# Optimization experiments

Hardware: AMD Instinct MI355X
Metric: run time of the kernel (lower is better)

Reference implementation:

```python
import jax, jax.numpy as jnp
import numpy as np
import math

# Config (matches init_kwargs)
V, D, L, H, KVH, FF = 4054, 1024, 8, 16, 8, 4096
HD = D // H            # 64
NREP = H // KVH        # 2
THETA = 500000.0
EPS = 1e-5
PAD = 4053
B, S = 2, 2048


def setup_inputs() -> dict:
    key = jax.random.key(0)
    ks = jax.random.split(key, 12)
    std = 0.02
    inp = {
        "input_ids": jax.random.randint(ks[0], (B, S), 0, 4050),
        "emb": jax.random.normal(ks[1], (V, D), jnp.float32) * std,
        # Linear weights stored as [in, out] so y = x @ W
        "Wq": jax.random.normal(ks[2], (L, D, H * HD), jnp.float32) * std,
        "Wk": jax.random.normal(ks[3], (L, D, KVH * HD), jnp.float32) * std,
        "Wv": jax.random.normal(ks[4], (L, D, KVH * HD), jnp.float32) * std,
        "Wo": jax.random.normal(ks[5], (L, H * HD, D), jnp.float32) * std,
        "Wg": jax.random.normal(ks[6], (L, D, FF), jnp.float32) * std,
        "Wu": jax.random.normal(ks[7], (L, D, FF), jnp.float32) * std,
        "Wd": jax.random.normal(ks[8], (L, FF, D), jnp.float32) * std,
        "attn_norm_w": jnp.ones((L, D), jnp.float32),
        "ffn_norm_w": jnp.ones((L, D), jnp.float32),
        "final_norm_w": jnp.ones((D,), jnp.float32),
        "lm_head": jax.random.normal(ks[9], (D, V), jnp.float32) * std,
    }
    return inp


def _rms_norm(x, w):
    return x * jax.lax.rsqrt(jnp.mean(x * x, axis=-1, keepdims=True) + EPS) * w


def _rotate_half(x):
    x1, x2 = jnp.split(x, 2, axis=-1)
    return jnp.concatenate([-x2, x1], axis=-1)


def _rope_tables(seq_len):
    inv_freq = 1.0 / (THETA ** (jnp.arange(0, HD, 2, dtype=jnp.float32) / HD))
    t = jnp.arange(seq_len, dtype=jnp.float32)
    freqs = jnp.outer(t, inv_freq)            # [S, HD/2]
    ang = jnp.concatenate([freqs, freqs], -1)  # [S, HD]
    return jnp.cos(ang)[None, None], jnp.sin(ang)[None, None]  # [1,1,S,HD]


def reference(input_ids, emb, Wq, Wk, Wv, Wo, Wg, Wu, Wd,
              attn_norm_w, ffn_norm_w, final_norm_w, lm_head):
    b, s = input_ids.shape
    x = emb[input_ids]                                    # [B,S,D]

    cos, sin = _rope_tables(s)

    # causal mask + pad-key mask (pad tokens cannot be attended to)
    causal = jnp.triu(jnp.full((s, s), -jnp.inf, jnp.float32), k=1)
    pad_bias = jnp.where(input_ids == PAD, -jnp.inf, 0.0)  # [B,S]
    mask = causal[None, None] + pad_bias[:, None, None, :]  # [B,1,S,S]

    scale = 1.0 / math.sqrt(HD)

    def block(h, p):
        wq, wk, wv, wo, wg, wu, wd, anw, fnw = p
        hn = _rms_norm(h, anw)
        q = (hn @ wq).reshape(b, s, H, HD).transpose(0, 2, 1, 3)    # [B,H,S,hd]
        k = (hn @ wk).reshape(b, s, KVH, HD).transpose(0, 2, 1, 3)  # [B,KVH,S,hd]
        v = (hn @ wv).reshape(b, s, KVH, HD).transpose(0, 2, 1, 3)
        q = q * cos + _rotate_half(q) * sin
        k = k * cos + _rotate_half(k) * sin
        k = jnp.repeat(k, NREP, axis=1)  # GQA expand -> [B,H,S,hd]
        v = jnp.repeat(v, NREP, axis=1)
        scores = jnp.einsum('bhqd,bhkd->bhqk', q, k) * scale + mask  # fp32
        attn = jax.nn.softmax(scores, axis=-1)
        o = jnp.einsum('bhqk,bhkd->bhqd', attn, v)
        o = o.transpose(0, 2, 1, 3).reshape(b, s, H * HD)
        h = h + o @ wo
        hn = _rms_norm(h, fnw)
        h = h + (jax.nn.silu(hn @ wg) * (hn @ wu)) @ wd
        return h, None

    x, _ = jax.lax.scan(block, x, (Wq, Wk, Wv, Wo, Wg, Wu, Wd, attn_norm_w, ffn_norm_w))
    logits = _rms_norm(x, final_norm_w) @ lm_head          # [B,S,V]
    return logits
```

## Files before the change

### kernel.cpp

```cpp
#include <hip/hip_runtime.h>

constexpr int C_NTOK = 4096;
constexpr int C_DIM  = 1024;
constexpr int C_NL   = 8;
constexpr int C_NH   = 16;
constexpr int C_NKVH = 8;
constexpr int C_FF   = 4096;
constexpr int C_HD   = 64;
constexpr int C_B    = 2;
constexpr int C_S    = 2048;
constexpr int C_V    = 4054;
constexpr int C_PAD  = 4053;

typedef unsigned short u16;
typedef unsigned int   u32;
typedef __attribute__((ext_vector_type(4))) float f32x4;
typedef __attribute__((ext_vector_type(8))) short s16x8;

__device__ __forceinline__ float bf2f(u16 u) {
  u32 i = ((u32)u) << 16; float f; __builtin_memcpy(&f, &i, 4); return f;
}
__device__ __forceinline__ u16 f2bf(float f) {
  u32 i; __builtin_memcpy(&i, &f, 4);
  return (u16)((i + 0x7FFFu + ((i >> 16) & 1u)) >> 16);
}
__device__ __forceinline__ f32x4 mfma16(s16x8 a, s16x8 b, f32x4 c) {
  return __builtin_amdgcn_mfma_f32_16x16x32_bf16(a, b, c, 0, 0, 0);
}
__device__ __forceinline__ void gld16(const void* g, void* l) {
  __builtin_amdgcn_global_load_lds((const __attribute__((address_space(1))) unsigned int*)g,
                                   (__attribute__((address_space(3))) unsigned int*)l, 16, 0, 0);
}

__global__ __launch_bounds__(256) void k_embed(const int* __restrict__ ids,
                                               const float* __restrict__ emb,
                                               float* __restrict__ x) {
  int t = blockIdx.x;
  const float4* src = (const float4*)(emb + (size_t)ids[t] * C_DIM);
  float4* dst = (float4*)(x + (size_t)t * C_DIM);
  dst[threadIdx.x] = src[threadIdx.x];
}

__global__ void k_bias(const int* __restrict__ ids, float* __restrict__ bias) {
  int i = blockIdx.x * 256 + threadIdx.x;
  if (i < C_NTOK) bias[i] = (ids[i] == C_PAD) ? -1e30f : 0.0f;
}

__global__ __launch_bounds__(256) void k_rmsnorm(const float* __restrict__ x,
                                                 const float* __restrict__ w,
                                                 u16* __restrict__ out) {
  int row = blockIdx.x, tid = threadIdx.x;
  float4 v = ((const float4*)(x + (size_t)row * C_DIM))[tid];
  float ss = v.x * v.x + v.y * v.y + v.z * v.z + v.w * v.w;
#pragma unroll
  for (int d = 1; d < 64; d <<= 1) ss += __shfl_xor(ss, d, 64);
  __shared__ float sm[4];
  if ((tid & 63) == 0) sm[tid >> 6] = ss;
  __syncthreads();
  float tot = sm[0] + sm[1] + sm[2] + sm[3];
  float rs = 1.0f / sqrtf(tot * (1.0f / C_DIM) + 1e-5f);
  float4 wv = ((const float4*)w)[tid];
  uint2 o;
  o.x = (u32)f2bf(v.x * rs * wv.x) | ((u32)f2bf(v.y * rs * wv.y) << 16);
  o.y = (u32)f2bf(v.z * rs * wv.z) | ((u32)f2bf(v.w * rs * wv.w) << 16);
  ((uint2*)(out + (size_t)row * C_DIM))[tid] = o;
}

__global__ __launch_bounds__(256) void k_wT(const float* __restrict__ W,
                                            u16* __restrict__ Wt,
                                            int K, int N, size_t szW, size_t szWt) {
  __shared__ u16 T[64][72];
  W  += (size_t)blockIdx.z * szW;
  Wt += (size_t)blockIdx.z * szWt;
  const int n0 = blockIdx.x * 64, k0 = blockIdx.y * 64;
  const int tid = threadIdx.x;
  const int r = tid >> 4, c4 = (tid & 15) * 4;
  const bool vec = ((N & 3) == 0);
#pragma unroll
  for (int it = 0; it < 4; ++it) {
    int k = k0 + r + it * 16;
    int n = n0 + c4;
    float4 v;
    if (vec && (n + 3 < N)) {
      v = *(const float4*)&W[(size_t)k * N + n];
    } else {
      v.x = (n + 0 < N) ? W[(size_t)k * N + n + 0] : 0.f;
      v.y = (n + 1 < N) ? W[(size_t)k * N + n + 1] : 0.f;
      v.z = (n + 2 < N) ? W[(size_t)k * N + n + 2] : 0.f;
      v.w = (n + 3 < N) ? W[(size_t)k * N + n + 3] : 0.f;
    }
    T[c4 + 0][r + it * 16] = f2bf(v.x);
    T[c4 + 1][r + it * 16] = f2bf(v.y);
    T[c4 + 2][r + it * 16] = f2bf(v.z);
    T[c4 + 3][r + it * 16] = f2bf(v.w);
  }
  __syncthreads();
  const int rr = tid >> 3, cc = (tid & 7) * 8;
#pragma unroll
  for (int jt = 0; jt < 2; ++jt) {
    int n = rr + jt * 32;
    *(uint4*)&Wt[(size_t)(n0 + n) * K + k0 + cc] = *(const uint4*)&T[n][cc];
  }
}

template <int EPI, int NS>
__global__ __launch_bounds__(256) void k_gemm(const u16* __restrict__ A,
                                              const u16* __restrict__ Bt,
                                              void* __restrict__ Cp,
                                              int N, int K, int lda) {
  __shared__ u16 As[2][128 * 32];
  __shared__ u16 Bs[2][128 * 32];
  const int nx = gridDim.x;
  int lin = blockIdx.y * nx + blockIdx.x;
  const int nwg = nx * gridDim.y;
  if ((nwg & 7) == 0) lin = (lin & 7) * (nwg >> 3) + (lin >> 3);
  const int bm = (lin / nx) * 128, bn = (lin % nx) * 128;
  const int tid = threadIdx.x;
  const int lane = tid & 63, wid = tid >> 6;
  const int wr = wid >> 1, wc = wid & 1;
  const int l16 = lane & 15, lg = lane >> 4;
  const int srow = tid >> 2, scol = (tid & 3) * 8;
  const u16* Ab = A + (size_t)(bm + srow) * lda + scol;
  const u16* Bb = Bt + (size_t)(bn + srow) * K + scol;
  const int kchunk = K / NS;
  const int kb0 = blockIdx.z * kchunk, kb1 = kb0 + kchunk;
  f32x4 acc[4][4] = {};
  {
    u16* ad = &As[0][tid * 8];
    u16* bd = &Bs[0][tid * 8];
    gld16(Ab + kb0, ad);
    gld16(Ab + (size_t)64 * lda + kb0, ad + 2048);
    gld16(Bb + kb0, bd);
    gld16(Bb + (size_t)64 * K + kb0, bd + 2048);
  }
  __syncthreads();
  int cur = 0;
  for (int kb = kb0; kb < kb1; kb += 32) {
    const int nkb = kb + 32;
    if (nkb < kb1) {
      u16* ad = &As[cur ^ 1][tid * 8];
      u16* bd = &Bs[cur ^ 1][tid * 8];
      gld16(Ab + nkb, ad);
      gld16(Ab + (size_t)64 * lda + nkb, ad + 2048);
      gld16(Bb + nkb, bd);
      gld16(Bb + (size_t)64 * K + nkb, bd + 2048);
    }
    s16x8 af[4], bfr[4];
#pragma unroll
    for (int i = 0; i < 4; ++i)
      af[i] = *(const s16x8*)&As[cur][(64 * wr + 16 * i + l16) * 32 + 8 * lg];
#pragma unroll
    for (int i = 0; i < 4; ++i)
      bfr[i] = *(const s16x8*)&Bs[cur][(64 * wc + 16 * i + l16) * 32 + 8 * lg];
#pragma unroll
    for (int mi = 0; mi < 4; ++mi)
#pragma unroll
      for (int ni = 0; ni < 4; ++ni)
        acc[mi][ni] = mfma16(af[mi], bfr[ni], acc[mi][ni]);
    __syncthreads();
    cur ^= 1;
  }
#pragma unroll
  for (int mi = 0; mi < 4; ++mi)
#pragma unroll
    for (int ni = 0; ni < 4; ++ni)
#pragma unroll
      for (int r = 0; r < 4; ++r) {
        int row = bm + 64 * wr + 16 * mi + 4 * lg + r;
        int col = bn + 64 * wc + 16 * ni + l16;
        if (col >= N) continue;
        float val = acc[mi][ni][r];
        size_t off = (size_t)row * N + col;
        if (EPI == 0)      ((u16*)Cp)[off] = f2bf(val);
        else if (EPI == 1) ((float*)Cp)[off] = val;
        else if (NS == 1)  ((float*)Cp)[off] += val;
        else               unsafeAtomicAdd((float*)Cp + off, val);
      }
}

__global__ void k_rope(u16* __restrict__ buf) {
  int idx = blockIdx.x * 256 + threadIdx.x;
  int j = idx & 15;
  int h = (idx >> 4) % 24;
  int t = idx / (16 * 24);
  int pos = t & (C_S - 1);
  const float L = 13.122363377404328f;
  float inv0 = expf(-(float)(4 * j)     * (1.0f / C_HD) * L);
  float inv1 = expf(-(float)(4 * j + 2) * (1.0f / C_HD) * L);
  float a0 = (float)pos * inv0, a1 = (float)pos * inv1;
  float c0 = cosf(a0), s0 = sinf(a0), c1 = cosf(a1), s1 = sinf(a1);
  int hoff = (h < 16) ? h * C_HD : 1024 + (h - 16) * C_HD;
  u16* pp = buf + (size_t)t * 2048 + hoff + 2 * j;
  u32 lo = *(u32*)pp;
  u32 hi = *(u32*)(pp + 32);
  float x0a = bf2f((u16)lo), x0b = bf2f((u16)(lo >> 16));
  float x1a = bf2f((u16)hi), x1b = bf2f((u16)(hi >> 16));
  *(u32*)pp        = (u32)f2bf(x0a * c0 - x1a * s0) | ((u32)f2bf(x0b * c1 - x1b * s1) << 16);
  *(u32*)(pp + 32) = (u32)f2bf(x1a * c0 + x0a * s0) | ((u32)f2bf(x1b * c1 + x0b * s1) << 16);
}

__global__ __launch_bounds__(256) void k_vT(const u16* __restrict__ qkv, u16* __restrict__ vt) {
  __shared__ u16 T[64][72];
  const int s0 = blockIdx.x * 64, kvh = blockIdx.y, b = blockIdx.z;
  const int tid = threadIdx.x;
  {
    const int r = tid >> 2, q = tid & 3;
    const u16* src = qkv + ((size_t)(b * C_S + s0 + r)) * 2048 + 1536 + kvh * C_HD + 16 * q;
    *(uint4*)&T[r][16 * q]     = *(const uint4*)src;
    *(uint4*)&T[r][16 * q + 8] = *(const uint4*)(src + 8);
  }
  __syncthreads();
  {
    const int hd = tid >> 2, sc4 = (tid & 3) * 16;
    u16 tmp[16];
#pragma unroll
    for (int jj = 0; jj < 16; ++jj) tmp[jj] = T[sc4 + jj][hd];
    u16* dst = vt + ((size_t)((b * C_NKVH + kvh) * C_HD + hd)) * C_S + s0 + sc4;
    *(uint4*)dst       = ((uint4*)tmp)[0];
    *(uint4*)(dst + 8) = ((uint4*)tmp)[1];
  }
}

__global__ __launch_bounds__(256) void k_pack(const u16* __restrict__ qkv,
                                              const u16* __restrict__ vt,
                                              u16* __restrict__ KP,
                                              u16* __restrict__ VP) {
  const int t = blockIdx.x, kvh = blockIdx.y, b = blockIdx.z;
  const int tid = threadIdx.x;
  const int lane = tid & 63, i4 = tid >> 6;
  const int l16 = lane & 15, lg = lane >> 4;
  const size_t obase = (((size_t)((b * 8 + kvh) * 32 + t)) * 8) * 512 + (size_t)lane * 8;
#pragma unroll
  for (int r = 0; r < 2; ++r) {
    int inst = i4 + 4 * r;
    int jt = inst >> 1, h = inst & 1;
    const u16* ks = qkv + (size_t)(b * C_S + 64 * t + 16 * jt + l16) * 2048
                    + 1024 + kvh * C_HD + 32 * h + 8 * lg;
    *(uint4*)(KP + obase + (size_t)inst * 512) = *(const uint4*)ks;
    const u16* vs = vt + ((size_t)((b * C_NKVH + kvh) * C_HD) + 16 * jt + l16) * C_S
                    + 64 * t + 32 * h + 8 * lg;
    *(uint4*)(VP + obase + (size_t)inst * 512) = *(const uint4*)vs;
  }
}

__global__ __launch_bounds__(64) void k_attn(const u16* __restrict__ qkv,
                                             const u16* __restrict__ KP,
                                             const u16* __restrict__ VP,
                                             const float* __restrict__ bias,
                                             u16* __restrict__ o) {
  const int qp = blockIdx.x, h = blockIdx.y, b = blockIdx.z;
  const int kvh = h >> 1;
  const int lane = threadIdx.x;
  const int l16 = lane & 15, lg = lane >> 4;
  __shared__ u16 P[16][72];
  const float* biasb = bias + b * C_S;
  const u16* kpb = KP + ((size_t)((b * 8 + kvh) * 32) * 8) * 512 + (size_t)lane * 8;
  const u16* vpb = VP + ((size_t)((b * 8 + kvh) * 32) * 8) * 512 + (size_t)lane * 8;
#pragma unroll
  for (int half = 0; half < 2; ++half) {
    const int qt = half ? (127 - qp) : qp;
    const int q0 = qt * 16;
    const int qrow = q0 + l16;
    const u16* qbase = qkv + (size_t)(b * C_S + qrow) * 2048 + h * C_HD + 8 * lg;
    s16x8 qf0 = *(const s16x8*)qbase;
    s16x8 qf1 = *(const s16x8*)(qbase + 32);
    float m = -1e30f, lsum = 0.f;
    f32x4 accO[4];
#pragma unroll
    for (int f = 0; f < 4; ++f) accO[f] = (f32x4){0.f, 0.f, 0.f, 0.f};
    const int nt = (q0 + 16 + 63) >> 6;
    s16x8 kf[8], vf[8];
#pragma unroll
    for (int i = 0; i < 8; ++i) kf[i] = *(const s16x8*)(kpb + (size_t)i * 512);
#pragma unroll
    for (int i = 0; i < 8; ++i) vf[i] = *(const s16x8*)(vpb + (size_t)i * 512);
    for (int t = 0; t < nt; ++t) {
      const int kt = t * 64;
      f32x4 sc[4];
#pragma unroll
      for (int jt = 0; jt < 4; ++jt) sc[jt] = (f32x4){0.f, 0.f, 0.f, 0.f};
#pragma unroll
      for (int jt = 0; jt < 4; ++jt) {
        sc[jt] = mfma16(kf[2 * jt],     qf0, sc[jt]);
        sc[jt] = mfma16(kf[2 * jt + 1], qf1, sc[jt]);
      }
      if (t + 1 < nt) {
        const u16* kn = kpb + (size_t)(t + 1) * 8 * 512;
#pragma unroll
        for (int i = 0; i < 8; ++i) kf[i] = *(const s16x8*)(kn + (size_t)i * 512);
      }
      float mt = -1e30f;
#pragma unroll
      for (int jt = 0; jt < 4; ++jt) {
        float4 bb = *(const float4*)&biasb[kt + 16 * jt + 4 * lg];
        int kv0 = kt + 16 * jt + 4 * lg;
        const float* bp = (const float*)&bb;
#pragma unroll
        for (int r = 0; r < 4; ++r) {
          float val = sc[jt][r] * 0.125f + bp[r];
          if (kv0 + r > qrow) val = -1e30f;
          sc[jt][r] = val;
          mt = fmaxf(mt, val);
        }
      }
      mt = fmaxf(mt, __shfl_xor(mt, 16, 64));
      mt = fmaxf(mt, __shfl_xor(mt, 32, 64));
      float mn = fmaxf(m, mt);
      float cc = __expf(m - mn);
      m = mn;
      float ps = 0.f;
#pragma unroll
      for (int jt = 0; jt < 4; ++jt)
#pragma unroll
        for (int r = 0; r < 4; ++r) {
          float pv = __expf(sc[jt][r] - m);
          sc[jt][r] = pv;
          ps += pv;
        }
      ps += __shfl_xor(ps, 16, 64);
      ps += __shfl_xor(ps, 32, 64);
      lsum = lsum * cc + ps;
#pragma unroll
      for (int f = 0; f < 4; ++f)
#pragma unroll
        for (int r = 0; r < 4; ++r) accO[f][r] *= cc;
#pragma unroll
      for (int jt = 0; jt < 4; ++jt) {
        uint2 w;
        w.x = (u32)f2bf(sc[jt][0]) | ((u32)f2bf(sc[jt][1]) << 16);
        w.y = (u32)f2bf(sc[jt][2]) | ((u32)f2bf(sc[jt][3]) << 16);
        *(uint2*)&P[l16][16 * jt + 4 * lg] = w;
      }
      asm volatile("s_waitcnt lgkmcnt(0)" ::: "memory");
      __builtin_amdgcn_sched_barrier(0);
      s16x8 pf0 = *(const s16x8*)&P[l16][8 * lg];
      s16x8 pf1 = *(const s16x8*)&P[l16][32 + 8 * lg];
#pragma unroll
      for (int f = 0; f < 4; ++f) {
        accO[f] = mfma16(vf[2 * f],     pf0, accO[f]);
        accO[f] = mfma16(vf[2 * f + 1], pf1, accO[f]);
      }
      if (t + 1 < nt) {
        const u16* vn = vpb + (size_t)(t + 1) * 8 * 512;
#pragma unroll
        for (int i = 0; i < 8; ++i) vf[i] = *(const s16x8*)(vn + (size_t)i * 512);
      }
    }
    float linv = 1.0f / lsum;
    u16* ob = o + ((size_t)(b * C_S + qrow)) * 1024 + h * C_HD + 4 * lg;
#pragma unroll
    for (int f = 0; f < 4; ++f) {
      uint2 w;
      w.x = (u32)f2bf(accO[f][0] * linv) | ((u32)f2bf(accO[f][1] * linv) << 16);
      w.y = (u32)f2bf(accO[f][2] * linv) | ((u32)f2bf(accO[f][3] * linv) << 16);
      *(uint2*)(ob + 16 * f) = w;
    }
  }
}

__global__ void k_silumul(u16* __restrict__ gu) {
  int idx = blockIdx.x * 256 + threadIdx.x;
  int row = idx >> 9;
  int c8 = (idx & 511) * 8;
  u16* g = gu + (size_t)row * 8192 + c8;
  const u16* u = g + 4096;
  uint4 gv = *(const uint4*)g;
  uint4 uv = *(const uint4*)u;
  u32* gp = (u32*)&gv;
  u32* up = (u32*)&uv;
  u32 go[4];
#pragma unroll
  for (int j = 0; j < 4; ++j) {
    float g0 = bf2f((u16)(gp[j] & 0xffff)), g1 = bf2f((u16)(gp[j] >> 16));
    float u0 = bf2f((u16)(up[j] & 0xffff)), u1 = bf2f((u16)(up[j] >> 16));
    float s0 = g0 / (1.0f + __expf(-g0));
    float s1 = g1 / (1.0f + __expf(-g1));
    go[j] = (u32)f2bf(s0 * u0) | ((u32)f2bf(s1 * u1) << 16);
  }
  *(uint4*)g = *(uint4*)go;
}

extern "C" void kernel_launch(void* const* d_in, const int* in_sizes, int n_in,
                              void* d_out, int out_size, void* d_ws, size_t ws_size,
                              hipStream_t stream) {
  const int*   ids  = (const int*)d_in[0];
  const float* emb  = (const float*)d_in[1];
  const float* Wq   = (const float*)d_in[2];
  const float* Wk   = (const float*)d_in[3];
  const float* Wv   = (const float*)d_in[4];
  const float* Wo   = (const float*)d_in[5];
  const float* Wg   = (const float*)d_in[6];
  const float* Wu   = (const float*)d_in[7];
  const float* Wd   = (const float*)d_in[8];
  const float* anw  = (const float*)d_in[9];
  const float* fnw  = (const float*)d_in[10];
  const float* finw = (const float*)d_in[11];
  const float* lmh  = (const float*)d_in[12];

  char* p = (char*)d_ws;
  float* x  = (float*)p; p += (size_t)C_NTOK * C_DIM * 4;
  u16* hn   = (u16*)p;   p += (size_t)C_NTOK * C_DIM * 2;
  u16* qkv  = (u16*)p;   p += (size_t)C_NTOK * 2048 * 2;
  u16* vtb  = (u16*)p;   p += (size_t)C_NTOK * C_NKVH * C_HD * 2;
  u16* ao   = (u16*)p;   p += (size_t)C_NTOK * C_NH * C_HD * 2;
  u16* gu   = (u16*)p;   p += (size_t)C_NTOK * 2 * C_FF * 2;
  u16* wT   = (u16*)p;   p += (size_t)8192 * 1024 * 2;
  float* bias = (float*)p; p += (size_t)C_NTOK * 4;
  u16* KP   = (u16*)p;   p += (size_t)C_B * 8 * 32 * 8 * 512 * 2;
  u16* VP   = (u16*)p;   p += (size_t)C_B * 8 * 32 * 8 * 512 * 2;
  u16* wTall = (u16*)p;

  const size_t M1 = 1024 * 1024;
  const size_t O_qkv = 0;
  const size_t O_wo  = O_qkv + 16 * M1;
  const size_t O_gu  = O_wo + 8 * M1;
  const size_t O_wd  = O_gu + 64 * M1;
  const size_t O_lmh = O_wd + 32 * M1;
  const size_t wTall_elems = O_lmh + 4 * M1;
  const size_t needed = ((char*)wTall - (char*)d_ws) + wTall_elems * 2;
  const bool big = ws_size >= needed;

  k_embed<<<C_NTOK, 256, 0, stream>>>(ids, emb, x);
  k_bias<<<C_NTOK / 256, 256, 0, stream>>>(ids, bias);

  if (big) {
    k_wT<<<dim3(16, 16, 8), 256, 0, stream>>>(Wq, wTall + O_qkv, C_DIM, 1024, M1, 2 * M1);
    k_wT<<<dim3(8, 16, 8), 256, 0, stream>>>(Wk, wTall + O_qkv + M1, C_DIM, 512, M1 / 2, 2 * M1);
    k_wT<<<dim3(8, 16, 8), 256, 0, stream>>>(Wv, wTall + O_qkv + M1 + M1 / 2, C_DIM, 512, M1 / 2, 2 * M1);
    k_wT<<<dim3(16, 16, 8), 256, 0, stream>>>(Wo, wTall + O_wo, 1024, C_DIM, M1, M1);
    k_wT<<<dim3(64, 16, 8), 256, 0, stream>>>(Wg, wTall + O_gu, C_DIM, C_FF, 4 * M1, 8 * M1);
    k_wT<<<dim3(64, 16, 8), 256, 0, stream>>>(Wu, wTall + O_gu + 4 * M1, C_DIM, C_FF, 4 * M1, 8 * M1);
    k_wT<<<dim3(16, 64, 8), 256, 0, stream>>>(Wd, wTall + O_wd, C_FF, C_DIM, 4 * M1, 4 * M1);
    k_wT<<<dim3(64, 16, 1), 256, 0, stream>>>(lmh, wTall + O_lmh, C_DIM, C_V, 0, 0);
  }

  for (int l = 0; l < C_NL; ++l) {
    k_rmsnorm<<<C_NTOK, 256, 0, stream>>>(x, anw + (size_t)l * C_DIM, hn);
    const u16* qkvT;
    if (big) {
      qkvT = wTall + O_qkv + (size_t)l * 2 * M1;
    } else {
      k_wT<<<dim3(16, 16), 256, 0, stream>>>(Wq + (size_t)l * M1, wT, C_DIM, 1024, 0, 0);
      k_wT<<<dim3(8, 16), 256, 0, stream>>>(Wk + (size_t)l * M1 / 2, wT + M1, C_DIM, 512, 0, 0);
      k_wT<<<dim3(8, 16), 256, 0, stream>>>(Wv + (size_t)l * M1 / 2, wT + M1 + M1 / 2, C_DIM, 512, 0, 0);
      qkvT = wT;
    }
    k_gemm<0, 1><<<dim3(16, 32), 256, 0, stream>>>(hn, qkvT, qkv, 2048, C_DIM, C_DIM);
    k_rope<<<C_NTOK * 24 * 16 / 256, 256, 0, stream>>>(qkv);
    k_vT<<<dim3(C_S / 64, C_NKVH, C_B), 256, 0, stream>>>(qkv, vtb);
    k_pack<<<dim3(32, C_NKVH, C_B), 256, 0, stream>>>(qkv, vtb, KP, VP);
    k_attn<<<dim3(64, C_NH, C_B), 64, 0, stream>>>(qkv, KP, VP, bias, ao);
    const u16* woT;
    if (big) {
      woT = wTall + O_wo + (size_t)l * M1;
    } else {
      k_wT<<<dim3(16, 16), 256, 0, stream>>>(Wo + (size_t)l * M1, wT, 1024, C_DIM, 0, 0);
      woT = wT;
    }
    k_gemm<2, 2><<<dim3(8, 32, 2), 256, 0, stream>>>(ao, woT, x, C_DIM, 1024, 1024);
    k_rmsnorm<<<C_NTOK, 256, 0, stream>>>(x, fnw + (size_t)l * C_DIM, hn);
    const u16* guT;
    if (big) {
      guT = wTall + O_gu + (size_t)l * 8 * M1;
    } else {
      k_wT<<<dim3(64, 16), 256, 0, stream>>>(Wg + (size_t)l * 4 * M1, wT, C_DIM, C_FF, 0, 0);
      k_wT<<<dim3(64, 16), 256, 0, stream>>>(Wu + (size_t)l * 4 * M1, wT + 4 * M1, C_DIM, C_FF, 0, 0);
      guT = wT;
    }
    k_gemm<0, 1><<<dim3(64, 32), 256, 0, stream>>>(hn, guT, gu, 8192, C_DIM, C_DIM);
    k_silumul<<<C_NTOK * 512 / 256, 256, 0, stream>>>(gu);
    const u16* wdT;
    if (big) {
      wdT = wTall + O_wd + (size_t)l * 4 * M1;
    } else {
      k_wT<<<dim3(16, 64), 256, 0, stream>>>(Wd + (size_t)l * 4 * M1, wT, C_FF, C_DIM, 0, 0);
      wdT = wT;
    }
    k_gemm<2, 4><<<dim3(8, 32, 4), 256, 0, stream>>>(gu, wdT, x, C_DIM, C_FF, 8192);
  }
  k_rmsnorm<<<C_NTOK, 256, 0, stream>>>(x, finw, hn);
  const u16* lmhT;
  if (big) {
    lmhT = wTall + O_lmh;
  } else {
    k_wT<<<dim3(64, 16), 256, 0, stream>>>(lmh, wT, C_DIM, C_V, 0, 0);
    lmhT = wT;
  }
  k_gemm<1, 1><<<dim3(32, 32), 256, 0, stream>>>(hn, lmhT, (float*)d_out, C_V, C_DIM, C_DIM);
}
```

Before: 3.033 ms.

## Add 256x256-tile double-buffered GEMM for gate/up and lm_head projections

Adds a new 512-thread GEMM kernel with 256x256 output tiles, double-buffered LDS staging with swizzled layout, and interleaved prefetch and MFMA phases with priority hints. It replaces the 128-tile GEMM for the fused gate/up projection and the final lm_head projection, aiming for more operand reuse per LDS load and better overlap of global loads with compute. The large LDS footprint limits occupancy. For lm_head, the kernel reads weight rows past the vocab size up to the padded tile width and relies on the column guard at the store.

```diff
diff --git a/kernel.cpp b/kernel.cpp
--- a/kernel.cpp
+++ b/kernel.cpp
@@ -178,6 +178,151 @@
       }
 }
 
+template <int EPI>
+__global__ __launch_bounds__(512, 2) void k_gemm256(const u16* __restrict__ A,
+                                                    const u16* __restrict__ Bt,
+                                                    void* __restrict__ Cp,
+                                                    int N, int K, int lda, int Nst) {
+  __shared__ u16 As[2][16384];
+  __shared__ u16 Bs[2][16384];
+  const int nx = gridDim.x;
+  int lin = blockIdx.y * nx + blockIdx.x;
+  const int nwg = nx * gridDim.y;
+  if ((nwg & 7) == 0) lin = (lin & 7) * (nwg >> 3) + (lin >> 3);
+  const int bm = (lin / nx) * 256, bn = (lin % nx) * 256;
+  const int tid = threadIdx.x;
+  const int lane = tid & 63, wid = tid >> 6;
+  const int wr = wid >> 2, wc = wid & 3;
+  const int l16 = lane & 15, lg = lane >> 4;
+  const int srow = tid >> 3;
+  const int scol = ((tid & 7) << 3) ^ (((tid >> 5) & 1) << 4);
+  const u16* Ab = A + (size_t)(bm + srow) * lda + scol;
+  const u16* Bb = Bt + (size_t)(bn + srow) * K + scol;
+  const int NT = K >> 6;
+  f32x4 acc[8][4] = {};
+
+#define STG_A(b, i, kt) gld16(Ab + (size_t)((i) * 64) * lda + (kt), &As[b][(i) * 4096 + tid * 8])
+#define STG_B(b, i, kt) gld16(Bb + (size_t)((i) * 64) * K + (kt), &Bs[b][(i) * 4096 + tid * 8])
+#define STG_HALF(b, h, kt)                                     \
+  do {                                                         \
+    if ((h) == 0)      { STG_A(b, 0, kt); STG_A(b, 1, kt); }   \
+    else if ((h) == 1) { STG_A(b, 2, kt); STG_A(b, 3, kt); }   \
+    else if ((h) == 2) { STG_B(b, 0, kt); STG_B(b, 1, kt); }   \
+    else               { STG_B(b, 2, kt); STG_B(b, 3, kt); }   \
+  } while (0)
+#define RD_FRAG(arr, b, row, kh)                                                    \
+  (*(const s16x8*)((const char*)&arr[b][0] +                                        \
+                   ((((row) << 7) + ((kh) << 6) + (lg << 4)) ^ ((((row) >> 2) & 1) << 5))))
+
+  STG_HALF(0, 0, 0); STG_HALF(0, 1, 0); STG_HALF(0, 2, 0); STG_HALF(0, 3, 0);
+  int c = 0;
+  for (int j = 0; j < NT; ++j) {
+    const int ktn = (j + 1) << 6;
+    const bool pf = (j + 1 < NT);
+    s16x8 af[4][2], bfr[4][2];
+    if (pf) { STG_HALF(c ^ 1, 0, ktn); asm volatile("s_waitcnt vmcnt(2)" ::: "memory"); }
+    else    { asm volatile("s_waitcnt vmcnt(0)" ::: "memory"); }
+    __builtin_amdgcn_s_barrier();
+    __builtin_amdgcn_sched_barrier(0);
+#pragma unroll
+    for (int i = 0; i < 4; ++i) {
+      int row = wr * 128 + i * 16 + l16;
+      af[i][0] = RD_FRAG(As, c, row, 0);
+      af[i][1] = RD_FRAG(As, c, row, 1);
+    }
+#pragma unroll
+    for (int n = 0; n < 2; ++n) {
+      int row = wc * 64 + n * 16 + l16;
+      bfr[n][0] = RD_FRAG(Bs, c, row, 0);
+      bfr[n][1] = RD_FRAG(Bs, c, row, 1);
+    }
+    asm volatile("s_waitcnt lgkmcnt(0)" ::: "memory");
+    __builtin_amdgcn_sched_barrier(0);
+    __builtin_amdgcn_s_setprio(1);
+#pragma unroll
+    for (int i = 0; i < 4; ++i)
+#pragma unroll
+      for (int n = 0; n < 2; ++n) {
+        acc[i][n] = mfma16(af[i][0], bfr[n][0], acc[i][n]);
+        acc[i][n] = mfma16(af[i][1], bfr[n][1], acc[i][n]);
+      }
+    __builtin_amdgcn_s_setprio(0);
+    __builtin_amdgcn_s_barrier();
+#pragma unroll
+    for (int n = 0; n < 2; ++n) {
+      int row = wc * 64 + (2 + n) * 16 + l16;
+      bfr[2 + n][0] = RD_FRAG(Bs, c, row, 0);
+      bfr[2 + n][1] = RD_FRAG(Bs, c, row, 1);
+    }
+    if (pf) STG_HALF(c ^ 1, 1, ktn);
+    __builtin_amdgcn_s_barrier();
+    asm volatile("s_waitcnt lgkmcnt(0)" ::: "memory");
+    __builtin_amdgcn_sched_barrier(0);
+    __builtin_amdgcn_s_setprio(1);
+#pragma unroll
+    for (int i = 0; i < 4; ++i)
+#pragma unroll
+      for (int n = 0; n < 2; ++n) {
+        acc[i][2 + n] = mfma16(af[i][0], bfr[2 + n][0], acc[i][2 + n]);
+        acc[i][2 + n] = mfma16(af[i][1], bfr[2 + n][1], acc[i][2 + n]);
+      }
+    __builtin_amdgcn_s_setprio(0);
+    __builtin_amdgcn_s_barrier();
+#pragma unroll
+    for (int i = 0; i < 4; ++i) {
+      int row = wr * 128 + (4 + i) * 16 + l16;
+      af[i][0] = RD_FRAG(As, c, row, 0);
+      af[i][1] = RD_FRAG(As, c, row, 1);
+    }
+    if (pf) STG_HALF(c ^ 1, 2, ktn);
+    __builtin_amdgcn_s_barrier();
+    asm volatile("s_waitcnt lgkmcnt(0)" ::: "memory");
+    __builtin_amdgcn_sched_barrier(0);
+    __builtin_amdgcn_s_setprio(1);
+#pragma unroll
+    for (int i = 0; i < 4; ++i)
+#pragma unroll
+      for (int n = 0; n < 2; ++n) {
+        acc[4 + i][n] = mfma16(af[i][0], bfr[n][0], acc[4 + i][n]);
+        acc[4 + i][n] = mfma16(af[i][1], bfr[n][1], acc[4 + i][n]);
+      }
+    __builtin_amdgcn_s_setprio(0);
+    __builtin_amdgcn_s_barrier();
+    if (pf) STG_HALF(c ^ 1, 3, ktn);
+    __builtin_amdgcn_s_barrier();
+    __builtin_amdgcn_s_setprio(1);
+#pragma unroll
+    for (int i = 0; i < 4; ++i)
+#pragma unroll
+      for (int n = 0; n < 2; ++n) {
+        acc[4 + i][2 + n] = mfma16(af[i][0], bfr[2 + n][0], acc[4 + i][2 + n]);
+        acc[4 + i][2 + n] = mfma16(af[i][1], bfr[2 + n][1], acc[4 + i][2 + n]);
+      }
+    __builtin_amdgcn_s_setprio(0);
+    __builtin_amdgcn_s_barrier();
+    c ^= 1;
+  }
+#undef STG_A
+#undef STG_B
+#undef STG_HALF
+#undef RD_FRAG
+#pragma unroll
+  for (int mi = 0; mi < 8; ++mi)
+#pragma unroll
+    for (int ni = 0; ni < 4; ++ni)
+#pragma unroll
+      for (int r = 0; r < 4; ++r) {
+        int row = bm + wr * 128 + mi * 16 + 4 * lg + r;
+        int col = bn + wc * 64 + ni * 16 + l16;
+        float val = acc[mi][ni][r];
+        if (EPI == 0) {
+          ((u16*)Cp)[(size_t)row * N + col] = f2bf(val);
+        } else {
+          if (col < Nst) ((float*)Cp)[(size_t)row * Nst + col] = val;
+        }
+      }
+}
+
 __global__ void k_rope(u16* __restrict__ buf) {
   int idx = blockIdx.x * 256 + threadIdx.x;
   int j = idx & 15;
@@ -467,7 +612,7 @@
       k_wT<<<dim3(64, 16), 256, 0, stream>>>(Wu + (size_t)l * 4 * M1, wT + 4 * M1, C_DIM, C_FF, 0, 0);
       guT = wT;
     }
-    k_gemm<0, 1><<<dim3(64, 32), 256, 0, stream>>>(hn, guT, gu, 8192, C_DIM, C_DIM);
+    k_gemm256<0><<<dim3(32, 16), 512, 0, stream>>>(hn, guT, gu, 8192, C_DIM, C_DIM, 8192);
     k_silumul<<<C_NTOK * 512 / 256, 256, 0, stream>>>(gu);
     const u16* wdT;
     if (big) {
@@ -486,5 +631,5 @@
     k_wT<<<dim3(64, 16), 256, 0, stream>>>(lmh, wT, C_DIM, C_V, 0, 0);
     lmhT = wT;
   }
-  k_gemm<1, 1><<<dim3(32, 32), 256, 0, stream>>>(hn, lmhT, (float*)d_out, C_V, C_DIM, C_DIM);
-}
+  k_gemm256<1><<<dim3(16, 16), 512, 0, stream>>>(hn, lmhT, d_out, 4096, C_DIM, C_DIM, C_V);
+}
```

Measured after the change: 2.947 ms. 2.8% less time.
